# Performance work log

Hardware: AMD Instinct MI355X
Metric: run time of the kernel (lower is better)

## Reference

```python
import jax, jax.numpy as jnp
import numpy as np

D_K = 8192   # sequence length (module calls it d_k)
D_MODEL = 128

def setup_inputs() -> dict:
    key = jax.random.key(0)
    k1, k2, k3 = jax.random.split(key, 3)
    Q = jax.random.normal(k1, (D_K, D_MODEL), dtype=jnp.float32)
    K = jax.random.normal(k2, (D_K, D_MODEL), dtype=jnp.float32)
    V = jax.random.normal(k3, (D_K, D_MODEL), dtype=jnp.float32)
    return {"Q": Q, "K": K, "V": V}

def reference(Q, K, V):
    # scores: [d_k, d_k] -- full attention matrix, scaled by 1/sqrt(d_k)
    # (faithful to the source: scale uses d_k, the sequence dim)
    inv_scale = 1.0 / jnp.sqrt(jnp.asarray(D_K, dtype=Q.dtype))
    scores = jnp.einsum('qd,kd->qk', Q, K) * inv_scale
    attn = jax.nn.softmax(scores, axis=-1)
    return jnp.einsum('qk,kd->qd', attn, V)
```

## Files before the change

kernel.cpp:

```cpp
#include <hip/hip_runtime.h>

#define SEQ 8192
#define DM  128
#define NKS 8

typedef __attribute__((ext_vector_type(8)))  short bf16x8;
typedef __attribute__((ext_vector_type(16))) float f32x16;

static __device__ __forceinline__ unsigned short f2bf(float f) {
    unsigned int u = __builtin_bit_cast(unsigned int, f);
    u += 0x7FFFu + ((u >> 16) & 1u);
    return (unsigned short)(u >> 16);
}
static __device__ __forceinline__ unsigned int pack2bf(float a, float b) {
    return ((unsigned int)f2bf(b) << 16) | (unsigned int)f2bf(a);
}
static __device__ __forceinline__ float bflo(unsigned int u) {
    return __builtin_bit_cast(float, u << 16);
}
static __device__ __forceinline__ float bfhi(unsigned int u) {
    return __builtin_bit_cast(float, u & 0xFFFF0000u);
}
static __device__ __forceinline__ bf16x8 as_frag(uint4 v) {
    return __builtin_bit_cast(bf16x8, v);
}
static __device__ __forceinline__ unsigned int pack2bf_trunc(float a, float b) {
    return __builtin_amdgcn_perm(__builtin_bit_cast(unsigned int, b),
                                 __builtin_bit_cast(unsigned int, a), 0x07060302u);
}
static __device__ __forceinline__ void gl_lds16(const void* g, void* l) {
    __builtin_amdgcn_global_load_lds(
        (const __attribute__((address_space(1))) void*)(unsigned long long)g,
        (__attribute__((address_space(3))) void*)(unsigned int)(unsigned long long)l,
        16, 0, 0);
}
#define CL2 (1.4426950408889634f / 90.50966799187809f)

__global__ __launch_bounds__(256) void prep_kernel(
        const float* __restrict__ Q, const float* __restrict__ K,
        const float* __restrict__ V,
        uint4* __restrict__ Qt, uint4* __restrict__ KV) {
    __shared__ float TL[32 * 136];
    const int b = blockIdx.x, tid = threadIdx.x;
    const int which = b >> 8, tile = b & 255;
    const float4* S4 = (which == 0) ? (const float4*)Q
                     : (which == 1) ? (const float4*)K : (const float4*)V;
    #pragma unroll
    for (int u = 0; u < 4; ++u) {
        int f4 = u * 256 + tid;
        int k = f4 >> 5, c4 = f4 & 31;
        float4 v = S4[(size_t)tile * 1024 + f4];
        *(float4*)(TL + k * 136 + c4 * 4) = v;
    }
    __syncthreads();
    if (which < 2) {
        const float scale = (which == 0) ? (float)CL2 : 1.0f;
        uint4* dst = (which == 0) ? (Qt + (size_t)tile * 512)
                                  : (KV + (size_t)tile * 1024);
        #pragma unroll
        for (int u = 0; u < 2; ++u) {
            int p = u * 256 + tid;
            int q = p & 31, h = (p >> 5) & 1, s = p >> 6;
            const float* src = TL + q * 136 + s * 16 + h * 8;
            float4 a = *(const float4*)(src);
            float4 c = *(const float4*)(src + 4);
            dst[p] = make_uint4(pack2bf(a.x * scale, a.y * scale),
                                pack2bf(a.z * scale, a.w * scale),
                                pack2bf(c.x * scale, c.y * scale),
                                pack2bf(c.z * scale, c.w * scale));
        }
    } else {
        uint4* dst = KV + (size_t)tile * 1024 + 512;
        #pragma unroll
        for (int u = 0; u < 2; ++u) {
            int p = u * 256 + tid;
            int q = p & 31, h = (p >> 5) & 1, p64 = p >> 6;
            int d = (p64 >> 1) * 32 + q;
            int k0 = (p64 & 1) * 16 + h * 8;
            unsigned int r[4];
            #pragma unroll
            for (int jj = 0; jj < 4; ++jj)
                r[jj] = pack2bf(TL[(k0 + 2 * jj) * 136 + d],
                                TL[(k0 + 2 * jj + 1) * 136 + d]);
            dst[p] = make_uint4(r[0], r[1], r[2], r[3]);
        }
    }
}

__global__ __launch_bounds__(256, 2) void attn_kernel(
        const uint4* __restrict__ Qt, const uint4* __restrict__ KV,
        unsigned short* __restrict__ Opart, float* __restrict__ Lpart) {
    __shared__ __align__(16) uint4 kvbuf[2][2][1024];
    __shared__ float Lw[4][64];
    const int tid = threadIdx.x;
    const int w = tid >> 6, lane = tid & 63;
    const int q = lane & 31, h = lane >> 5;
    const int wq = w & 1, ss = w >> 1;
    const int ks = blockIdx.x & 7, qt = blockIdx.x >> 3;
    const int sub = qt * 2 + wq;

    uint4 qf0[8], qf1[8];
    {
        const uint4* qs = Qt + (size_t)(2 * sub) * 512 + lane;
        #pragma unroll
        for (int s = 0; s < 8; ++s) { qf0[s] = qs[s * 64]; qf1[s] = qs[512 + s * 64]; }
    }

    f32x16 oacc[8];
    #pragma unroll
    for (int a = 0; a < 8; ++a)
        #pragma unroll
        for (int r = 0; r < 16; ++r) oacc[a][r] = 0.f;
    float ls0 = 0.f, ls1 = 0.f;

    const uint4* kv0 = KV + ((size_t)(ks * 32 + ss * 16)) * 1024 + wq * 512;
    auto stage = [&](int buf, int t) {
        const uint4* src = kv0 + (size_t)t * 1024;
        uint4* dst = &kvbuf[ss][buf][wq * 512];
        #pragma unroll
        for (int u = 0; u < 8; ++u)
            gl_lds16(src + u * 64 + lane, dst + u * 64);
    };

    stage(0, 0);
    __syncthreads();
    #pragma unroll 1
    for (int t = 0; t < 16; ++t) {
        if (t < 15) stage((t + 1) & 1, t + 1);
        const uint4* kb = &kvbuf[ss][t & 1][0];

        f32x16 s0, s1;
        #pragma unroll
        for (int r = 0; r < 16; ++r) { s0[r] = 0.f; s1[r] = 0.f; }
        #pragma unroll
        for (int s = 0; s < 8; ++s) {
            uint4 kf = kb[s * 64 + lane];
            s0 = __builtin_amdgcn_mfma_f32_32x32x16_bf16(as_frag(kf), as_frag(qf0[s]), s0, 0, 0, 0);
            s1 = __builtin_amdgcn_mfma_f32_32x32x16_bf16(as_frag(kf), as_frag(qf1[s]), s1, 0, 0, 0);
        }

        #pragma unroll
        for (int g = 0; g < 2; ++g) {
            float p[16];
            #pragma unroll
            for (int r = 0; r < 16; ++r) {
                float sv = g ? s1[r] : s0[r];
                p[r] = __builtin_amdgcn_exp2f(sv);
                if (g) ls1 += p[r]; else ls0 += p[r];
            }
            unsigned int pk[8], px[8];
            #pragma unroll
            for (int jj = 0; jj < 8; ++jj) pk[jj] = pack2bf_trunc(p[2 * jj], p[2 * jj + 1]);
            #pragma unroll
            for (int jj = 0; jj < 8; ++jj) px[jj] = (unsigned int)__shfl_xor((int)pk[jj], 32);
            uint4 B0, B1;
            B0.x = h ? px[2] : pk[0];  B0.y = h ? px[3] : pk[1];
            B0.z = h ? pk[2] : px[0];  B0.w = h ? pk[3] : px[1];
            B1.x = h ? px[6] : pk[4];  B1.y = h ? px[7] : pk[5];
            B1.z = h ? pk[6] : px[4];  B1.w = h ? pk[7] : px[5];
            #pragma unroll
            for (int mb = 0; mb < 4; ++mb) {
                uint4 va = kb[512 + (2 * mb) * 64 + lane];
                uint4 vb = kb[512 + (2 * mb + 1) * 64 + lane];
                oacc[g * 4 + mb] = __builtin_amdgcn_mfma_f32_32x32x16_bf16(
                    as_frag(va), as_frag(B0), oacc[g * 4 + mb], 0, 0, 0);
                oacc[g * 4 + mb] = __builtin_amdgcn_mfma_f32_32x32x16_bf16(
                    as_frag(vb), as_frag(B1), oacc[g * 4 + mb], 0, 0, 0);
            }
        }
        __syncthreads();
    }

    float l0 = ls0 + __shfl_xor(ls0, 32);
    float l1 = ls1 + __shfl_xor(ls1, 32);
    if (h == 0) { Lw[w][q] = l0; Lw[w][32 + q] = l1; }
    if (w >= 2) {
        float* D = (float*)&kvbuf[0][0][0] + (w - 2) * 8192;
        #pragma unroll
        for (int a = 0; a < 8; ++a)
            #pragma unroll
            for (int r = 0; r < 16; ++r)
                D[(a * 16 + r) * 64 + lane] = oacc[a][r];
    }
    __syncthreads();
    if (w < 2) {
        const float* D = (const float*)&kvbuf[0][0][0] + w * 8192;
        #pragma unroll
        for (int a = 0; a < 8; ++a)
            #pragma unroll
            for (int r = 0; r < 16; ++r)
                oacc[a][r] += D[(a * 16 + r) * 64 + lane];
        if (h == 0) {
            Lpart[ks * SEQ + sub * 64 + q]      = l0 + Lw[w + 2][q];
            Lpart[ks * SEQ + sub * 64 + 32 + q] = l1 + Lw[w + 2][32 + q];
        }
        unsigned short* dst = Opart + ((size_t)(ks * 128 + sub)) * 8192 + lane * 16;
        #pragma unroll
        for (int a = 0; a < 8; ++a) {
            unsigned int o[8];
            #pragma unroll
            for (int u = 0; u < 8; ++u)
                o[u] = pack2bf(oacc[a][2 * u], oacc[a][2 * u + 1]);
            *(uint4*)(dst + a * 1024)     = make_uint4(o[0], o[1], o[2], o[3]);
            *(uint4*)(dst + a * 1024 + 8) = make_uint4(o[4], o[5], o[6], o[7]);
        }
    }
}

__global__ __launch_bounds__(256) void reduce_kernel(
        const unsigned short* __restrict__ Opart, const float* __restrict__ Lpart,
        float* __restrict__ Out) {
    __shared__ float T[64 * 132];
    __shared__ float Linv[64];
    const int tid = threadIdx.x, sub = blockIdx.x;
    if (tid < 64) {
        float L = 0.f;
        #pragma unroll
        for (int ks = 0; ks < NKS; ++ks) L += Lpart[ks * SEQ + sub * 64 + tid];
        Linv[tid] = 1.0f / L;
    }
    const int l = tid & 63, A = tid >> 6;
    float acc[32];
    #pragma unroll
    for (int u = 0; u < 32; ++u) acc[u] = 0.f;
    #pragma unroll 1
    for (int ks = 0; ks < NKS; ++ks) {
        const unsigned short* src = Opart + ((size_t)(ks * 128 + sub)) * 8192 + l * 16;
        #pragma unroll
        for (int ai = 0; ai < 2; ++ai) {
            const uint4* s4 = (const uint4*)(src + (2 * A + ai) * 1024);
            uint4 v0 = s4[0], v1 = *(const uint4*)((const unsigned short*)s4 + 8);
            float* a = acc + ai * 16;
            a[0] += bflo(v0.x);  a[1] += bfhi(v0.x);
            a[2] += bflo(v0.y);  a[3] += bfhi(v0.y);
            a[4] += bflo(v0.z);  a[5] += bfhi(v0.z);
            a[6] += bflo(v0.w);  a[7] += bfhi(v0.w);
            a[8] += bflo(v1.x);  a[9] += bfhi(v1.x);
            a[10] += bflo(v1.y); a[11] += bfhi(v1.y);
            a[12] += bflo(v1.z); a[13] += bfhi(v1.z);
            a[14] += bflo(v1.w); a[15] += bfhi(v1.w);
        }
    }
    const int hh = l >> 5;
    #pragma unroll
    for (int ai = 0; ai < 2; ++ai) {
        int a = 2 * A + ai;
        int q_loc = (a >> 2) * 32 + (l & 31);
        #pragma unroll
        for (int r = 0; r < 16; ++r) {
            int d = (a & 3) * 32 + (r & 3) + 8 * (r >> 2) + 4 * hh;
            T[q_loc * 132 + d] = acc[ai * 16 + r];
        }
    }
    __syncthreads();
    const int q_loc = tid >> 2, dseg = (tid & 3) * 32;
    const float rv = Linv[q_loc];
    #pragma unroll
    for (int c = 0; c < 8; ++c) {
        const float* tp = T + q_loc * 132 + dseg + c * 4;
        float4 o = make_float4(tp[0] * rv, tp[1] * rv, tp[2] * rv, tp[3] * rv);
        *(float4*)(Out + (size_t)(sub * 64 + q_loc) * DM + dseg + c * 4) = o;
    }
}

extern "C" void kernel_launch(void* const* d_in, const int* in_sizes, int n_in,
                              void* d_out, int out_size, void* d_ws, size_t ws_size,
                              hipStream_t stream) {
    const float* Q = (const float*)d_in[0];
    const float* K = (const float*)d_in[1];
    const float* V = (const float*)d_in[2];
    char* ws = (char*)d_ws;
    uint4* Qt            = (uint4*)ws;
    uint4* KV            = (uint4*)(ws + 2 * 1024 * 1024);
    float* Lpart         = (float*)(ws + 6 * 1024 * 1024);
    unsigned short* Opart= (unsigned short*)(ws + 6 * 1024 * 1024 + 262144);
    float* Out = (float*)d_out;

    prep_kernel<<<768, 256, 0, stream>>>(Q, K, V, Qt, KV);
    attn_kernel<<<512, 256, 0, stream>>>(Qt, KV, Opart, Lpart);
    reduce_kernel<<<128, 256, 0, stream>>>(Opart, Lpart, Out);
}
```

Measured before the change: 125.1 us.

## Fuse split-K reduction into attention kernel and convert Q on the fly

Drops the Q conversion from the prep kernel and instead loads fp32 Q directly in the attention kernel, scaling and packing it to bf16 in registers. Restructures the attention block so each wave owns 32 queries and walks 32 key tiles, with K staged through LDS and V read straight from global memory. The separate reduce kernel is removed: the last split block for each query tile, detected with an atomic counter, sums the partials and writes the output. This saves a kernel launch and the Q round trip through memory, in exchange for serialised tail work, uncached V loads and changed occupancy.

```diff
diff --git a/kernel.cpp b/kernel.cpp
--- a/kernel.cpp
+++ b/kernel.cpp
@@ -37,14 +37,13 @@
 #define CL2 (1.4426950408889634f / 90.50966799187809f)
 
 __global__ __launch_bounds__(256) void prep_kernel(
-        const float* __restrict__ Q, const float* __restrict__ K,
-        const float* __restrict__ V,
-        uint4* __restrict__ Qt, uint4* __restrict__ KV) {
+        const float* __restrict__ K, const float* __restrict__ V,
+        uint4* __restrict__ Kt, uint4* __restrict__ Vt, int* __restrict__ cnt) {
     __shared__ float TL[32 * 136];
     const int b = blockIdx.x, tid = threadIdx.x;
     const int which = b >> 8, tile = b & 255;
-    const float4* S4 = (which == 0) ? (const float4*)Q
-                     : (which == 1) ? (const float4*)K : (const float4*)V;
+    if (b == 0 && tid < 64) cnt[tid] = 0;
+    const float4* S4 = which ? (const float4*)V : (const float4*)K;
     #pragma unroll
     for (int u = 0; u < 4; ++u) {
         int f4 = u * 256 + tid;
@@ -53,10 +52,7 @@
         *(float4*)(TL + k * 136 + c4 * 4) = v;
     }
     __syncthreads();
-    if (which < 2) {
-        const float scale = (which == 0) ? (float)CL2 : 1.0f;
-        uint4* dst = (which == 0) ? (Qt + (size_t)tile * 512)
-                                  : (KV + (size_t)tile * 1024);
+    if (which == 0) {
         #pragma unroll
         for (int u = 0; u < 2; ++u) {
             int p = u * 256 + tid;
@@ -64,13 +60,10 @@
             const float* src = TL + q * 136 + s * 16 + h * 8;
             float4 a = *(const float4*)(src);
             float4 c = *(const float4*)(src + 4);
-            dst[p] = make_uint4(pack2bf(a.x * scale, a.y * scale),
-                                pack2bf(a.z * scale, a.w * scale),
-                                pack2bf(c.x * scale, c.y * scale),
-                                pack2bf(c.z * scale, c.w * scale));
+            Kt[(size_t)tile * 512 + p] = make_uint4(pack2bf(a.x, a.y), pack2bf(a.z, a.w),
+                                                    pack2bf(c.x, c.y), pack2bf(c.z, c.w));
         }
     } else {
-        uint4* dst = KV + (size_t)tile * 1024 + 512;
         #pragma unroll
         for (int u = 0; u < 2; ++u) {
             int p = u * 256 + tid;
@@ -82,121 +75,109 @@
             for (int jj = 0; jj < 4; ++jj)
                 r[jj] = pack2bf(TL[(k0 + 2 * jj) * 136 + d],
                                 TL[(k0 + 2 * jj + 1) * 136 + d]);
-            dst[p] = make_uint4(r[0], r[1], r[2], r[3]);
-        }
-    }
-}
-
-__global__ __launch_bounds__(256, 2) void attn_kernel(
-        const uint4* __restrict__ Qt, const uint4* __restrict__ KV,
-        unsigned short* __restrict__ Opart, float* __restrict__ Lpart) {
-    __shared__ __align__(16) uint4 kvbuf[2][2][1024];
-    __shared__ float Lw[4][64];
+            Vt[(size_t)tile * 512 + p] = make_uint4(r[0], r[1], r[2], r[3]);
+        }
+    }
+}
+
+__global__ __launch_bounds__(256) void attn_kernel(
+        const float* __restrict__ Q,
+        const uint4* __restrict__ Kt, const uint4* __restrict__ Vt,
+        unsigned short* __restrict__ Opart, float* __restrict__ Lpart,
+        int* __restrict__ cnt, float* __restrict__ Out) {
+    __shared__ __align__(16) char smem[17408];
+    __shared__ int redflag;
     const int tid = threadIdx.x;
-    const int w = tid >> 6, lane = tid & 63;
+    const int qg = tid >> 6, lane = tid & 63;
     const int q = lane & 31, h = lane >> 5;
-    const int wq = w & 1, ss = w >> 1;
     const int ks = blockIdx.x & 7, qt = blockIdx.x >> 3;
-    const int sub = qt * 2 + wq;
-
-    uint4 qf0[8], qf1[8];
+    const int qbase = qt * 128 + qg * 32;
+    const int tile0 = ks * 32;
+
+    uint4 qf[8];
     {
-        const uint4* qs = Qt + (size_t)(2 * sub) * 512 + lane;
-        #pragma unroll
-        for (int s = 0; s < 8; ++s) { qf0[s] = qs[s * 64]; qf1[s] = qs[512 + s * 64]; }
-    }
-
-    f32x16 oacc[8];
+        const float4* Qr = (const float4*)Q + (size_t)(qbase + q) * 32 + 2 * h;
+        #pragma unroll
+        for (int s = 0; s < 8; ++s) {
+            float4 a = Qr[4 * s], b = Qr[4 * s + 1];
+            qf[s] = make_uint4(pack2bf(a.x * CL2, a.y * CL2),
+                               pack2bf(a.z * CL2, a.w * CL2),
+                               pack2bf(b.x * CL2, b.y * CL2),
+                               pack2bf(b.z * CL2, b.w * CL2));
+        }
+    }
+
+    f32x16 oacc[4];
     #pragma unroll
-    for (int a = 0; a < 8; ++a)
+    for (int a = 0; a < 4; ++a)
         #pragma unroll
         for (int r = 0; r < 16; ++r) oacc[a][r] = 0.f;
-    float ls0 = 0.f, ls1 = 0.f;
-
-    const uint4* kv0 = KV + ((size_t)(ks * 32 + ss * 16)) * 1024 + wq * 512;
+    float lsum = 0.f;
+
     auto stage = [&](int buf, int t) {
-        const uint4* src = kv0 + (size_t)t * 1024;
-        uint4* dst = &kvbuf[ss][buf][wq * 512];
-        #pragma unroll
-        for (int u = 0; u < 8; ++u)
-            gl_lds16(src + u * 64 + lane, dst + u * 64);
+        const uint4* src = Kt + (size_t)(tile0 + t) * 512 + qg * 128 + lane;
+        gl_lds16(src,      smem + buf * 8192 + (qg * 2) * 1024);
+        gl_lds16(src + 64, smem + buf * 8192 + (qg * 2 + 1) * 1024);
     };
 
     stage(0, 0);
     __syncthreads();
     #pragma unroll 1
-    for (int t = 0; t < 16; ++t) {
-        if (t < 15) stage((t + 1) & 1, t + 1);
-        const uint4* kb = &kvbuf[ss][t & 1][0];
-
-        f32x16 s0, s1;
-        #pragma unroll
-        for (int r = 0; r < 16; ++r) { s0[r] = 0.f; s1[r] = 0.f; }
-        #pragma unroll
-        for (int s = 0; s < 8; ++s) {
-            uint4 kf = kb[s * 64 + lane];
-            s0 = __builtin_amdgcn_mfma_f32_32x32x16_bf16(as_frag(kf), as_frag(qf0[s]), s0, 0, 0, 0);
-            s1 = __builtin_amdgcn_mfma_f32_32x32x16_bf16(as_frag(kf), as_frag(qf1[s]), s1, 0, 0, 0);
-        }
-
-        #pragma unroll
-        for (int g = 0; g < 2; ++g) {
-            float p[16];
-            #pragma unroll
-            for (int r = 0; r < 16; ++r) {
-                float sv = g ? s1[r] : s0[r];
-                p[r] = __builtin_amdgcn_exp2f(sv);
-                if (g) ls1 += p[r]; else ls0 += p[r];
-            }
-            unsigned int pk[8], px[8];
-            #pragma unroll
-            for (int jj = 0; jj < 8; ++jj) pk[jj] = pack2bf_trunc(p[2 * jj], p[2 * jj + 1]);
-            #pragma unroll
-            for (int jj = 0; jj < 8; ++jj) px[jj] = (unsigned int)__shfl_xor((int)pk[jj], 32);
-            uint4 B0, B1;
-            B0.x = h ? px[2] : pk[0];  B0.y = h ? px[3] : pk[1];
-            B0.z = h ? pk[2] : px[0];  B0.w = h ? pk[3] : px[1];
-            B1.x = h ? px[6] : pk[4];  B1.y = h ? px[7] : pk[5];
-            B1.z = h ? pk[6] : px[4];  B1.w = h ? pk[7] : px[5];
-            #pragma unroll
-            for (int mb = 0; mb < 4; ++mb) {
-                uint4 va = kb[512 + (2 * mb) * 64 + lane];
-                uint4 vb = kb[512 + (2 * mb + 1) * 64 + lane];
-                oacc[g * 4 + mb] = __builtin_amdgcn_mfma_f32_32x32x16_bf16(
-                    as_frag(va), as_frag(B0), oacc[g * 4 + mb], 0, 0, 0);
-                oacc[g * 4 + mb] = __builtin_amdgcn_mfma_f32_32x32x16_bf16(
-                    as_frag(vb), as_frag(B1), oacc[g * 4 + mb], 0, 0, 0);
-            }
+    for (int t = 0; t < 32; ++t) {
+        if (t < 31) stage((t + 1) & 1, t + 1);
+        const char* kl = smem + (t & 1) * 8192 + lane * 16;
+
+        uint4 kf[8];
+        #pragma unroll
+        for (int s = 0; s < 8; ++s) kf[s] = *(const uint4*)(kl + s * 1024);
+
+        f32x16 sacc;
+        #pragma unroll
+        for (int r = 0; r < 16; ++r) sacc[r] = 0.f;
+        #pragma unroll
+        for (int s = 0; s < 8; ++s)
+            sacc = __builtin_amdgcn_mfma_f32_32x32x16_bf16(
+                       as_frag(kf[s]), as_frag(qf[s]), sacc, 0, 0, 0);
+
+        uint4 vf[8];
+        const uint4* vsrc = Vt + (size_t)(tile0 + t) * 512 + lane;
+        #pragma unroll
+        for (int w = 0; w < 8; ++w) vf[w] = vsrc[w * 64];
+
+        float p[16];
+        #pragma unroll
+        for (int r = 0; r < 16; ++r) {
+            p[r] = __builtin_amdgcn_exp2f(sacc[r]);
+            lsum += p[r];
+        }
+        unsigned int pk[8], px[8];
+        #pragma unroll
+        for (int jj = 0; jj < 8; ++jj) pk[jj] = pack2bf_trunc(p[2 * jj], p[2 * jj + 1]);
+        #pragma unroll
+        for (int jj = 0; jj < 8; ++jj) px[jj] = (unsigned int)__shfl_xor((int)pk[jj], 32);
+        uint4 B0, B1;
+        B0.x = h ? px[2] : pk[0];  B0.y = h ? px[3] : pk[1];
+        B0.z = h ? pk[2] : px[0];  B0.w = h ? pk[3] : px[1];
+        B1.x = h ? px[6] : pk[4];  B1.y = h ? px[7] : pk[5];
+        B1.z = h ? pk[6] : px[4];  B1.w = h ? pk[7] : px[5];
+
+        #pragma unroll
+        for (int mb = 0; mb < 4; ++mb) {
+            oacc[mb] = __builtin_amdgcn_mfma_f32_32x32x16_bf16(
+                           as_frag(vf[2 * mb]), as_frag(B0), oacc[mb], 0, 0, 0);
+            oacc[mb] = __builtin_amdgcn_mfma_f32_32x32x16_bf16(
+                           as_frag(vf[2 * mb + 1]), as_frag(B1), oacc[mb], 0, 0, 0);
         }
         __syncthreads();
     }
 
-    float l0 = ls0 + __shfl_xor(ls0, 32);
-    float l1 = ls1 + __shfl_xor(ls1, 32);
-    if (h == 0) { Lw[w][q] = l0; Lw[w][32 + q] = l1; }
-    if (w >= 2) {
-        float* D = (float*)&kvbuf[0][0][0] + (w - 2) * 8192;
-        #pragma unroll
-        for (int a = 0; a < 8; ++a)
-            #pragma unroll
-            for (int r = 0; r < 16; ++r)
-                D[(a * 16 + r) * 64 + lane] = oacc[a][r];
-    }
-    __syncthreads();
-    if (w < 2) {
-        const float* D = (const float*)&kvbuf[0][0][0] + w * 8192;
-        #pragma unroll
-        for (int a = 0; a < 8; ++a)
-            #pragma unroll
-            for (int r = 0; r < 16; ++r)
-                oacc[a][r] += D[(a * 16 + r) * 64 + lane];
-        if (h == 0) {
-            Lpart[ks * SEQ + sub * 64 + q]      = l0 + Lw[w + 2][q];
-            Lpart[ks * SEQ + sub * 64 + 32 + q] = l1 + Lw[w + 2][32 + q];
-        }
-        unsigned short* dst = Opart + ((size_t)(ks * 128 + sub)) * 8192 + lane * 16;
-        #pragma unroll
-        for (int a = 0; a < 8; ++a) {
+    float l2 = lsum + __shfl_xor(lsum, 32);
+    if (h == 0) Lpart[ks * SEQ + qbase + q] = l2;
+    {
+        unsigned short* dst = Opart + ((size_t)(ks * 256 + qt * 4 + qg)) * 4096
+                              + lane * 16;
+        #pragma unroll
+        for (int a = 0; a < 4; ++a) {
             unsigned int o[8];
             #pragma unroll
             for (int u = 0; u < 8; ++u)
@@ -205,61 +186,60 @@
             *(uint4*)(dst + a * 1024 + 8) = make_uint4(o[4], o[5], o[6], o[7]);
         }
     }
-}
-
-__global__ __launch_bounds__(256) void reduce_kernel(
-        const unsigned short* __restrict__ Opart, const float* __restrict__ Lpart,
-        float* __restrict__ Out) {
-    __shared__ float T[64 * 132];
-    __shared__ float Linv[64];
-    const int tid = threadIdx.x, sub = blockIdx.x;
-    if (tid < 64) {
-        float L = 0.f;
-        #pragma unroll
-        for (int ks = 0; ks < NKS; ++ks) L += Lpart[ks * SEQ + sub * 64 + tid];
-        Linv[tid] = 1.0f / L;
-    }
-    const int l = tid & 63, A = tid >> 6;
-    float acc[32];
-    #pragma unroll
-    for (int u = 0; u < 32; ++u) acc[u] = 0.f;
+    __threadfence();
+    __syncthreads();
+    if (tid == 0) redflag = (atomicAdd(&cnt[qt], 1) == NKS - 1);
+    __syncthreads();
+    if (!redflag) return;
+    __threadfence();
+
+    float* T    = (float*)smem;
+    float* Linv = (float*)(smem + 16896);
+    const int A = tid >> 6, l = tid & 63, hh = l >> 5, qq = l & 31;
     #pragma unroll 1
-    for (int ks = 0; ks < NKS; ++ks) {
-        const unsigned short* src = Opart + ((size_t)(ks * 128 + sub)) * 8192 + l * 16;
-        #pragma unroll
-        for (int ai = 0; ai < 2; ++ai) {
-            const uint4* s4 = (const uint4*)(src + (2 * A + ai) * 1024);
-            uint4 v0 = s4[0], v1 = *(const uint4*)((const unsigned short*)s4 + 8);
-            float* a = acc + ai * 16;
-            a[0] += bflo(v0.x);  a[1] += bfhi(v0.x);
-            a[2] += bflo(v0.y);  a[3] += bfhi(v0.y);
-            a[4] += bflo(v0.z);  a[5] += bfhi(v0.z);
-            a[6] += bflo(v0.w);  a[7] += bfhi(v0.w);
-            a[8] += bflo(v1.x);  a[9] += bfhi(v1.x);
-            a[10] += bflo(v1.y); a[11] += bfhi(v1.y);
-            a[12] += bflo(v1.z); a[13] += bfhi(v1.z);
-            a[14] += bflo(v1.w); a[15] += bfhi(v1.w);
-        }
-    }
-    const int hh = l >> 5;
-    #pragma unroll
-    for (int ai = 0; ai < 2; ++ai) {
-        int a = 2 * A + ai;
-        int q_loc = (a >> 2) * 32 + (l & 31);
+    for (int tq = 0; tq < 4; ++tq) {
+        const int tile_id = qt * 4 + tq;
+        float acc[16];
+        #pragma unroll
+        for (int r = 0; r < 16; ++r) acc[r] = 0.f;
+        #pragma unroll 1
+        for (int k2 = 0; k2 < NKS; ++k2) {
+            const uint4* s4 = (const uint4*)(Opart
+                + ((size_t)(k2 * 256 + tile_id)) * 4096 + A * 1024 + l * 16);
+            uint4 v0 = s4[0], v1 = s4[1];
+            acc[0] += bflo(v0.x);  acc[1] += bfhi(v0.x);
+            acc[2] += bflo(v0.y);  acc[3] += bfhi(v0.y);
+            acc[4] += bflo(v0.z);  acc[5] += bfhi(v0.z);
+            acc[6] += bflo(v0.w);  acc[7] += bfhi(v0.w);
+            acc[8] += bflo(v1.x);  acc[9] += bfhi(v1.x);
+            acc[10] += bflo(v1.y); acc[11] += bfhi(v1.y);
+            acc[12] += bflo(v1.z); acc[13] += bfhi(v1.z);
+            acc[14] += bflo(v1.w); acc[15] += bfhi(v1.w);
+        }
+        if (tid < 32) {
+            float L = 0.f;
+            #pragma unroll
+            for (int k2 = 0; k2 < NKS; ++k2)
+                L += Lpart[k2 * SEQ + qt * 128 + tq * 32 + tid];
+            Linv[tid] = 1.0f / L;
+        }
         #pragma unroll
         for (int r = 0; r < 16; ++r) {
-            int d = (a & 3) * 32 + (r & 3) + 8 * (r >> 2) + 4 * hh;
-            T[q_loc * 132 + d] = acc[ai * 16 + r];
-        }
-    }
-    __syncthreads();
-    const int q_loc = tid >> 2, dseg = (tid & 3) * 32;
-    const float rv = Linv[q_loc];
-    #pragma unroll
-    for (int c = 0; c < 8; ++c) {
-        const float* tp = T + q_loc * 132 + dseg + c * 4;
-        float4 o = make_float4(tp[0] * rv, tp[1] * rv, tp[2] * rv, tp[3] * rv);
-        *(float4*)(Out + (size_t)(sub * 64 + q_loc) * DM + dseg + c * 4) = o;
+            int d = A * 32 + (r & 3) + 8 * (r >> 2) + 4 * hh;
+            T[d * 33 + qq] = acc[r];
+        }
+        __syncthreads();
+        const int row = tid >> 3, seg = (tid & 7) * 16;
+        const float rv = Linv[row];
+        #pragma unroll
+        for (int e = 0; e < 16; e += 4) {
+            float4 o = make_float4(T[(seg + e + 0) * 33 + row] * rv,
+                                   T[(seg + e + 1) * 33 + row] * rv,
+                                   T[(seg + e + 2) * 33 + row] * rv,
+                                   T[(seg + e + 3) * 33 + row] * rv);
+            *(float4*)(Out + (size_t)(tile_id * 32 + row) * DM + seg + e) = o;
+        }
+        __syncthreads();
     }
 }
 
@@ -270,13 +250,13 @@
     const float* K = (const float*)d_in[1];
     const float* V = (const float*)d_in[2];
     char* ws = (char*)d_ws;
-    uint4* Qt            = (uint4*)ws;
-    uint4* KV            = (uint4*)(ws + 2 * 1024 * 1024);
-    float* Lpart         = (float*)(ws + 6 * 1024 * 1024);
-    unsigned short* Opart= (unsigned short*)(ws + 6 * 1024 * 1024 + 262144);
+    uint4* Kt            = (uint4*)ws;
+    uint4* Vt            = (uint4*)(ws + 2 * 1024 * 1024);
+    float* Lpart         = (float*)(ws + 4 * 1024 * 1024);
+    int*   cnt           = (int*)(ws + 4 * 1024 * 1024 + 262144);
+    unsigned short* Opart= (unsigned short*)(ws + 4 * 1024 * 1024 + 262144 + 1024);
     float* Out = (float*)d_out;
 
-    prep_kernel<<<768, 256, 0, stream>>>(Q, K, V, Qt, KV);
-    attn_kernel<<<512, 256, 0, stream>>>(Qt, KV, Opart, Lpart);
-    reduce_kernel<<<128, 256, 0, stream>>>(Opart, Lpart, Out);
-}
+    prep_kernel<<<512, 256, 0, stream>>>(K, V, Kt, Vt, cnt);
+    attn_kernel<<<512, 256, 0, stream>>>(Q, Kt, Vt, Opart, Lpart, cnt, Out);
+}
```

Result: slower. 211.7 us (+69.2%).
